# Optimization experiments

Measured on AMD Instinct MI355X. Metric: run time of the kernel, lower is better.

The kernel has to match this reference:

```python
import jax, jax.numpy as jnp
from jax import lax
import numpy as np

T, B, N_INP = 512, 128, 128
N_HID, N_CH, N_OUT, KSIZE = 1024, 2, 10, 3


def setup_inputs() -> dict:
    key = jax.random.key(0)
    ks = jax.random.split(key, 5)
    x = jax.random.normal(ks[0], (T, B, N_INP), jnp.float32)
    # Wx: Linear(n_inp, n_hid*n_ch); original inits std=0.001, scale similarly
    Wx_w = jax.random.normal(ks[1], (N_HID * N_CH, N_INP), jnp.float32) * 0.001
    Wx_b = jnp.zeros((N_HID * N_CH,), jnp.float32)
    # LocallyConnected1d weight [out_ch, in_ch, n_hid, ksize] (leading 1 squeezed)
    Wy_w = jax.random.normal(ks[2], (N_CH, N_CH, N_HID, KSIZE), jnp.float32) * (1.0 / np.sqrt(N_CH * KSIZE))
    Wy_b = jnp.zeros((N_CH, N_HID), jnp.float32)
    R_w = jax.random.normal(ks[3], (N_OUT, N_HID * N_CH), jnp.float32) * (1.0 / np.sqrt(N_HID * N_CH))
    R_b = jnp.zeros((N_OUT,), jnp.float32)
    return {"x": x, "Wx_w": Wx_w, "Wx_b": Wx_b, "Wy_w": Wy_w, "Wy_b": Wy_b, "R_w": R_w, "R_b": R_b}


def reference(x, Wx_w, Wx_b, Wy_w, Wy_b, R_w, R_b):
    n_ch, _, n_hid, ksize = Wy_w.shape
    p = ksize // 2
    # window indices into circularly padded hidden axis (length n_hid + 2p)
    widx = jnp.arange(n_hid)[:, None] + jnp.arange(ksize)[None, :]

    def step(hy, xt):
        # encoder: [B, n_inp] @ [n_inp, n_hid*n_ch]
        u = xt @ Wx_w.T + Wx_b
        h = hy.reshape(-1, n_ch, n_hid)
        # circular pad along hidden dim
        hp = jnp.concatenate([h[..., -p:], h, h[..., :p]], axis=-1)
        win = hp[..., widx]  # [B, n_ch, n_hid, ksize]
        loc = jnp.einsum('bchk,ochk->boh', win, Wy_w) + Wy_b  # [B, n_ch, n_hid]
        hy_new = jnp.tanh(u + loc.reshape(hy.shape[0], n_ch * n_hid))
        return hy_new, None

    hy0 = jnp.zeros((x.shape[1], n_ch * n_hid), x.dtype)
    hy, _ = lax.scan(step, hy0, x)
    return hy @ R_w.T + R_b  # [B, n_out]
```

## Files before the change

### kernel.cpp

```cpp
#include <hip/hip_runtime.h>
#include <hip/hip_bf16.h>

#define T_TOT 512
#define NB    128
#define NI    128
#define NH    1024
#define NJ    2048

typedef __attribute__((ext_vector_type(8))) short short8;
typedef __attribute__((ext_vector_type(4))) float f32x4;
typedef __attribute__((ext_vector_type(2))) float f32x2;

__device__ __forceinline__ unsigned short f2bf_u(float f) {
  __hip_bfloat16 h = __float2bfloat16(f);
  unsigned short s; __builtin_memcpy(&s, &h, 2); return s;
}
__device__ __forceinline__ float bf2f(unsigned short u) {
  unsigned v = ((unsigned)u) << 16; float f; __builtin_memcpy(&f, &v, 4); return f;
}

__global__ void cvt_wx(const float* __restrict__ w,
                       unsigned short* __restrict__ hi,
                       unsigned short* __restrict__ lo) {
  int i = blockIdx.x * blockDim.x + threadIdx.x;
  for (int k = i; k < NJ * NI; k += gridDim.x * blockDim.x) {
    float f = w[k];
    unsigned short h = f2bf_u(f);
    hi[k] = h;
    lo[k] = f2bf_u(f - bf2f(h));
  }
}

__global__ void cvt_x(const float* __restrict__ x,
                      unsigned short* __restrict__ hi,
                      unsigned short* __restrict__ lo) {
  const int n = T_TOT * NB * NI;
  int i = blockIdx.x * blockDim.x + threadIdx.x;
  for (int k = i; k < n; k += gridDim.x * blockDim.x) {
    float f = x[k];
    unsigned short h = f2bf_u(f);
    hi[k] = h;
    lo[k] = f2bf_u(f - bf2f(h));
  }
}

#define MFMA __builtin_amdgcn_mfma_f32_16x16x32_bf16

__global__ __launch_bounds__(256) void fused(
    const unsigned short* __restrict__ xhi,
    const unsigned short* __restrict__ xlo,
    const unsigned short* __restrict__ Whi,
    const unsigned short* __restrict__ Wlo,
    const float* __restrict__ Wxb,
    float* __restrict__ Uw,
    const float* __restrict__ Ur,
    const float* __restrict__ Wyw,
    const float* __restrict__ Wyb,
    const float* __restrict__ Rw,
    const float* __restrict__ Rb,
    float* __restrict__ state,
    float* __restrict__ out,
    int T_c, int nrec, int flags)
{
  __shared__ float edge[2][2][4][2];
  __shared__ float red[4][10];

  if ((int)blockIdx.x < nrec) {
    __builtin_amdgcn_s_setprio(1);
    const int b    = blockIdx.x;
    const int tid  = threadIdx.x;
    const int lane = tid & 63;
    const int wv   = tid >> 6;
    const int n0   = tid * 4;

    f32x2 WP0[12], WP1[12], BP[4];
    {
      const float* w00 = Wyw + (size_t)n0 * 3;
      const float* w01 = Wyw + (size_t)(NH + n0) * 3;
      const float* w10 = Wyw + (size_t)(2 * NH + n0) * 3;
      const float* w11 = Wyw + (size_t)(3 * NH + n0) * 3;
      #pragma unroll
      for (int i = 0; i < 12; ++i) {
        f32x2 a = {w00[i], w10[i]}; WP0[i] = a;
        f32x2 c = {w01[i], w11[i]}; WP1[i] = c;
      }
      #pragma unroll
      for (int j = 0; j < 4; ++j) { f32x2 bb = {Wyb[n0 + j], Wyb[NH + n0 + j]}; BP[j] = bb; }
    }

    float y0[4], y1[4];
    if (flags & 1) {
      #pragma unroll
      for (int j = 0; j < 4; ++j) { y0[j] = 0.f; y1[j] = 0.f; }
    } else {
      float4 s0 = *(const float4*)(state + (size_t)b * NJ + n0);
      float4 s1 = *(const float4*)(state + (size_t)b * NJ + NH + n0);
      y0[0]=s0.x; y0[1]=s0.y; y0[2]=s0.z; y0[3]=s0.w;
      y1[0]=s1.x; y1[1]=s1.y; y1[2]=s1.z; y1[3]=s1.w;
    }

    float lv0, lv1, rv0, rv1;

#define EXCH(P) do {                                                          \
    if (lane == 0)  { edge[P][0][wv][0] = y0[0]; edge[P][0][wv][1] = y1[0]; } \
    if (lane == 63) { edge[P][1][wv][0] = y0[3]; edge[P][1][wv][1] = y1[3]; } \
    lv0 = __shfl(y0[3], (lane + 63) & 63);                                    \
    lv1 = __shfl(y1[3], (lane + 63) & 63);                                    \
    rv0 = __shfl(y0[0], (lane + 1) & 63);                                     \
    rv1 = __shfl(y1[0], (lane + 1) & 63);                                     \
    asm volatile("s_waitcnt lgkmcnt(0)" ::: "memory");                        \
    __builtin_amdgcn_s_barrier();                                             \
    if (lane == 0)  { lv0 = edge[P][1][(wv + 3) & 3][0]; lv1 = edge[P][1][(wv + 3) & 3][1]; } \
    if (lane == 63) { rv0 = edge[P][0][(wv + 1) & 3][0]; rv1 = edge[P][0][(wv + 1) & 3][1]; } \
  } while (0)

#define STEP(P, U0V, U1V) do {                                                \
    float h0[6], h1[6];                                                       \
    h0[0]=lv0; h0[1]=y0[0]; h0[2]=y0[1]; h0[3]=y0[2]; h0[4]=y0[3]; h0[5]=rv0; \
    h1[0]=lv1; h1[1]=y1[0]; h1[2]=y1[1]; h1[3]=y1[2]; h1[4]=y1[3]; h1[5]=rv1; \
    const float u0a[4] = {(U0V).x, (U0V).y, (U0V).z, (U0V).w};                \
    const float u1a[4] = {(U1V).x, (U1V).y, (U1V).z, (U1V).w};                \
    _Pragma("unroll")                                                         \
    for (int j = 0; j < 4; ++j) {                                             \
      f32x2 acc = BP[j];                                                      \
      f32x2 h;                                                                \
      h = (f32x2){h0[j],   h0[j]};   acc = __builtin_elementwise_fma(WP0[j*3+0], h, acc); \
      h = (f32x2){h0[j+1], h0[j+1]}; acc = __builtin_elementwise_fma(WP0[j*3+1], h, acc); \
      h = (f32x2){h0[j+2], h0[j+2]}; acc = __builtin_elementwise_fma(WP0[j*3+2], h, acc); \
      h = (f32x2){h1[j],   h1[j]};   acc = __builtin_elementwise_fma(WP1[j*3+0], h, acc); \
      h = (f32x2){h1[j+1], h1[j+1]}; acc = __builtin_elementwise_fma(WP1[j*3+1], h, acc); \
      h = (f32x2){h1[j+2], h1[j+2]}; acc = __builtin_elementwise_fma(WP1[j*3+2], h, acc); \
      acc += (f32x2){u0a[j], u1a[j]};                                         \
      f32x2 xx = acc * 2.88539008177792681f;   \
      float e0 = __builtin_amdgcn_exp2f(xx.x);                                \
      float e1 = __builtin_amdgcn_exp2f(xx.y);                                \
      y0[j] = fmaf(-2.0f, __builtin_amdgcn_rcpf(e0 + 1.0f), 1.0f);            \
      y1[j] = fmaf(-2.0f, __builtin_amdgcn_rcpf(e1 + 1.0f), 1.0f);            \
    }                                                                         \
    EXCH(P);                                                                  \
  } while (0)

    EXCH(1);

    const float* Ub = Ur + (size_t)b * NJ + n0;
#define LD(S, T) do { const size_t o = (size_t)(T) * ((size_t)NB * NJ);       \
    S##0 = *(const float4*)(Ub + o); S##1 = *(const float4*)(Ub + o + NH); } while (0)

    float4 pA0,pA1,pB0,pB1,pC0,pC1,pD0,pD1,pE0,pE1,pF0,pF1,pG0,pG1,pH0,pH1;
    LD(pA,0); LD(pB,1); LD(pC,2); LD(pD,3); LD(pE,4); LD(pF,5); LD(pG,6); LD(pH,7);

    for (int t = 0; t < T_c; t += 8) {
      STEP(0, pA0, pA1); if (t +  8 < T_c) LD(pA, t +  8);
      STEP(1, pB0, pB1); if (t +  9 < T_c) LD(pB, t +  9);
      STEP(0, pC0, pC1); if (t + 10 < T_c) LD(pC, t + 10);
      STEP(1, pD0, pD1); if (t + 11 < T_c) LD(pD, t + 11);
      STEP(0, pE0, pE1); if (t + 12 < T_c) LD(pE, t + 12);
      STEP(1, pF0, pF1); if (t + 13 < T_c) LD(pF, t + 13);
      STEP(0, pG0, pG1); if (t + 14 < T_c) LD(pG, t + 14);
      STEP(1, pH0, pH1); if (t + 15 < T_c) LD(pH, t + 15);
    }
#undef LD
#undef STEP
#undef EXCH

    if (flags & 2) {
      float p[10];
      #pragma unroll
      for (int r = 0; r < 10; ++r) {
        float4 ra = *(const float4*)(Rw + (size_t)r * NJ + n0);
        float4 rb = *(const float4*)(Rw + (size_t)r * NJ + NH + n0);
        p[r] = y0[0]*ra.x + y0[1]*ra.y + y0[2]*ra.z + y0[3]*ra.w
             + y1[0]*rb.x + y1[1]*rb.y + y1[2]*rb.z + y1[3]*rb.w;
      }
      #pragma unroll
      for (int r = 0; r < 10; ++r) {
        #pragma unroll
        for (int off = 32; off > 0; off >>= 1)
          p[r] += __shfl_down(p[r], off);
      }
      __syncthreads();
      if (lane == 0) {
        #pragma unroll
        for (int r = 0; r < 10; ++r) red[wv][r] = p[r];
      }
      __syncthreads();
      if (tid < 10)
        out[blockIdx.x * 10 + tid] = red[0][tid] + red[1][tid] + red[2][tid] + red[3][tid] + Rb[tid];
    } else {
      *(float4*)(state + (size_t)b * NJ + n0)      = make_float4(y0[0], y0[1], y0[2], y0[3]);
      *(float4*)(state + (size_t)b * NJ + NH + n0) = make_float4(y1[0], y1[1], y1[2], y1[3]);
    }
  } else {
    const int gb = blockIdx.x - nrec;
    const int ts = gb >> 2;
    const int q  = gb & 3;
    const int l  = threadIdx.x & 63;
    const int lr = l & 15;
    const int lk = l >> 4;
    const long m0 = (long)ts * 128 + (threadIdx.x >> 6) * 32;
    const int jb = q * (NJ / 4);

    short8 xh[2][4], xl[2][4];
    #pragma unroll
    for (int ms = 0; ms < 2; ++ms) {
      const size_t base = (size_t)(m0 + ms * 16 + lr) * NI + lk * 8;
      #pragma unroll
      for (int kk = 0; kk < 4; ++kk) {
        xh[ms][kk] = *(const short8*)(xhi + base + kk * 32);
        xl[ms][kk] = *(const short8*)(xlo + base + kk * 32);
      }
    }

#define LOADW(WH, WL, J0) do {                                                \
    const size_t wo = (size_t)((J0) + lr) * NI + lk * 8;                      \
    WH[0] = *(const short8*)(Whi + wo);       WH[1] = *(const short8*)(Whi + wo + 32); \
    WH[2] = *(const short8*)(Whi + wo + 64);  WH[3] = *(const short8*)(Whi + wo + 96); \
    WL[0] = *(const short8*)(Wlo + wo);       WL[1] = *(const short8*)(Wlo + wo + 32); \
    WL[2] = *(const short8*)(Wlo + wo + 64);  WL[3] = *(const short8*)(Wlo + wo + 96); \
  } while (0)

#define COMPUTE(WH, WL, J0) do {                                              \
    f32x4 acc0 = {0.f, 0.f, 0.f, 0.f};                                        \
    f32x4 acc1 = {0.f, 0.f, 0.f, 0.f};                                        \
    _Pragma("unroll")                                                         \
    for (int kk = 0; kk < 4; ++kk) {                                          \
      acc0 = MFMA(WH[kk], xh[0][kk], acc0, 0, 0, 0);                          \
      acc0 = MFMA(WH[kk], xl[0][kk], acc0, 0, 0, 0);                          \
      acc0 = MFMA(WL[kk], xh[0][kk], acc0, 0, 0, 0);                          \
      acc1 = MFMA(WH[kk], xh[1][kk], acc1, 0, 0, 0);                          \
      acc1 = MFMA(WH[kk], xl[1][kk], acc1, 0, 0, 0);                          \
      acc1 = MFMA(WL[kk], xh[1][kk], acc1, 0, 0, 0);                          \
    }                                                                         \
    const float4 b4 = *(const float4*)(Wxb + (J0) + lk * 4);                  \
    float4 o0 = make_float4(acc0[0] + b4.x, acc0[1] + b4.y, acc0[2] + b4.z, acc0[3] + b4.w); \
    float4 o1 = make_float4(acc1[0] + b4.x, acc1[1] + b4.y, acc1[2] + b4.z, acc1[3] + b4.w); \
    *(float4*)(Uw + (m0 + lr) * NJ + (J0) + lk * 4)        = o0;              \
    *(float4*)(Uw + (m0 + 16 + lr) * NJ + (J0) + lk * 4)   = o1;              \
  } while (0)

    short8 whA[4], wlA[4], whB[4], wlB[4];
    LOADW(whA, wlA, jb);
    for (int s = 0; s < 32; s += 2) {
      const int j0 = jb + s * 16;
      LOADW(whB, wlB, j0 + 16);
      COMPUTE(whA, wlA, j0);
      if (s + 2 < 32) LOADW(whA, wlA, j0 + 32);
      COMPUTE(whB, wlB, j0 + 16);
    }
#undef LOADW
#undef COMPUTE
  }
}

__global__ __launch_bounds__(1024) void recur_fb(
    const float* __restrict__ x,
    const float* __restrict__ Wxw, const float* __restrict__ Wxb,
    const float* __restrict__ Wyw, const float* __restrict__ Wyb,
    const float* __restrict__ Rw,  const float* __restrict__ Rb,
    float* __restrict__ out)
{
  const int b = blockIdx.x;
  const int n = threadIdx.x;
  __shared__ float2 h2[2][NH];
  __shared__ float  xs[NI];
  __shared__ float  red[16][10];

  const float w000 = Wyw[(size_t)n*3+0],        w001 = Wyw[(size_t)n*3+1],        w002 = Wyw[(size_t)n*3+2];
  const float w010 = Wyw[(size_t)(NH+n)*3+0],   w011 = Wyw[(size_t)(NH+n)*3+1],   w012 = Wyw[(size_t)(NH+n)*3+2];
  const float w100 = Wyw[(size_t)(2*NH+n)*3+0], w101 = Wyw[(size_t)(2*NH+n)*3+1], w102 = Wyw[(size_t)(2*NH+n)*3+2];
  const float w110 = Wyw[(size_t)(3*NH+n)*3+0], w111 = Wyw[(size_t)(3*NH+n)*3+1], w112 = Wyw[(size_t)(3*NH+n)*3+2];
  const float bias0 = Wyb[n], bias1 = Wyb[NH + n];
  const int nm1 = (n + NH - 1) & (NH - 1);
  const int np1 = (n + 1) & (NH - 1);

  float c0 = 0.f, c1 = 0.f;
  h2[0][n] = make_float2(c0, c1);
  __syncthreads();

  int cur = 0;
  for (int t = 0; t < T_TOT; ++t) {
    if (n < NI) xs[n] = x[(size_t)t * NB * NI + (size_t)b * NI + n];
    __syncthreads();
    float u0 = Wxb[n], u1 = Wxb[NH + n];
    const float* wr0 = Wxw + (size_t)n * NI;
    const float* wr1 = Wxw + (size_t)(NH + n) * NI;
    #pragma unroll 8
    for (int i = 0; i < NI; ++i) {
      u0 = fmaf(xs[i], wr0[i], u0);
      u1 = fmaf(xs[i], wr1[i], u1);
    }
    float2 Lv = h2[cur][nm1];
    float2 Rv = h2[cur][np1];
    float loc0 = bias0 + w000*Lv.x + w001*c0 + w002*Rv.x + w010*Lv.y + w011*c1 + w012*Rv.y;
    float loc1 = bias1 + w100*Lv.x + w101*c0 + w102*Rv.x + w110*Lv.y + w111*c1 + w112*Rv.y;
    float e0 = __expf(2.0f * (u0 + loc0));
    float e1 = __expf(2.0f * (u1 + loc1));
    c0 = 1.0f - __fdividef(2.0f, e0 + 1.0f);
    c1 = 1.0f - __fdividef(2.0f, e1 + 1.0f);
    h2[cur ^ 1][n] = make_float2(c0, c1);
    cur ^= 1;
    __syncthreads();
  }

  float p[10];
  #pragma unroll
  for (int r = 0; r < 10; ++r)
    p[r] = c0 * Rw[(size_t)r * NJ + n] + c1 * Rw[(size_t)r * NJ + NH + n];
  #pragma unroll
  for (int r = 0; r < 10; ++r) {
    #pragma unroll
    for (int off = 32; off > 0; off >>= 1)
      p[r] += __shfl_down(p[r], off);
  }
  const int wv = n >> 6;
  if ((n & 63) == 0) {
    #pragma unroll
    for (int r = 0; r < 10; ++r) red[wv][r] = p[r];
  }
  __syncthreads();
  if (n < 10) {
    float s = 0.f;
    #pragma unroll
    for (int k = 0; k < 16; ++k) s += red[k][n];
    out[b * 10 + n] = s + Rb[n];
  }
}

extern "C" void kernel_launch(void* const* d_in, const int* in_sizes, int n_in,
                              void* d_out, int out_size, void* d_ws, size_t ws_size,
                              hipStream_t stream) {
  const float* x   = (const float*)d_in[0];
  const float* Wxw = (const float*)d_in[1];
  const float* Wxb = (const float*)d_in[2];
  const float* Wyw = (const float*)d_in[3];
  const float* Wyb = (const float*)d_in[4];
  const float* Rw  = (const float*)d_in[5];
  const float* Rb  = (const float*)d_in[6];
  float* out = (float*)d_out;

  const size_t w1_bytes = (size_t)NJ * NI * 2;
  const size_t x1_bytes = (size_t)T_TOT * NB * NI * 2;
  const size_t st_bytes = (size_t)NB * NJ * 4;
  const size_t ut_bytes = (size_t)NB * NJ * 4;

  char* p = (char*)d_ws;
  unsigned short* Whi = (unsigned short*)p;              p += w1_bytes;
  unsigned short* Wlo = (unsigned short*)p;              p += w1_bytes;
  unsigned short* Xhi = (unsigned short*)p;              p += x1_bytes;
  unsigned short* Xlo = (unsigned short*)p;              p += x1_bytes;
  float* state = (float*)p;                              p += st_bytes;
  float* U     = (float*)p;
  const size_t fixed = (size_t)(p - (char*)d_ws);

  long Tc = 64;
  while (Tc >= 8 && fixed + 2 * (size_t)Tc * ut_bytes > ws_size) Tc >>= 1;

  if (Tc >= 8) {
    const int NC = T_TOT / (int)Tc;
    const size_t uhalf = (size_t)Tc * NB * NJ;
    cvt_wx<<<64, 256, 0, stream>>>(Wxw, Whi, Wlo);
    cvt_x<<<1024, 256, 0, stream>>>(x, Xhi, Xlo);
    fused<<<(int)Tc * 4, 256, 0, stream>>>(
        Xhi, Xlo, Whi, Wlo, Wxb, U, nullptr,
        Wyw, Wyb, Rw, Rb, state, out, (int)Tc, 0, 0);
    for (int i = 0; i < NC; ++i) {
      const int flags = (i == 0 ? 1 : 0) | (i == NC - 1 ? 2 : 0);
      const int ng = (i + 1 < NC) ? (int)Tc * 4 : 0;
      const size_t xo = (size_t)(i + 1) * Tc * NB * NI;
      fused<<<128 + ng, 256, 0, stream>>>(
          Xhi + (ng ? xo : 0), Xlo + (ng ? xo : 0), Whi, Wlo, Wxb,
          U + ((size_t)((i + 1) & 1)) * uhalf,
          U + ((size_t)(i & 1)) * uhalf,
          Wyw, Wyb, Rw, Rb, state, out, (int)Tc, 128, flags);
    }
  } else {
    recur_fb<<<NB, 1024, 0, stream>>>(x, Wxw, Wxb, Wyw, Wyb, Rw, Rb, out);
  }
}
```

Baseline: 410.9 us.

## Stage recurrent U prefetch through LDS ring via global_load_lds and split GEMM blocks finer

The recurrent blocks now prefetch the precomputed input projections into a 6-slot LDS ring using direct global-to-LDS loads with explicit vmcnt waits, instead of holding 8 timesteps of float4 registers. This aims to cut register pressure and keep more loads in flight ahead of the serial tanh recurrence. The concurrent GEMM producer blocks are split into 8 column chunks per timestep instead of 4, doubling their count with half the work each. The 48KB LDS ring lowers occupancy for all blocks, including the GEMM blocks that share the kernel, and the hand-written waitcnt counts must match the number of outstanding loads exactly.

After: 430.9 us. 4.9% more time.

```diff
diff --git a/kernel.cpp b/kernel.cpp
--- a/kernel.cpp
+++ b/kernel.cpp
@@ -1,11 +1,13 @@
 #include <hip/hip_runtime.h>
 #include <hip/hip_bf16.h>
+#include <stdint.h>
 
 #define T_TOT 512
 #define NB    128
 #define NI    128
 #define NH    1024
 #define NJ    2048
+#define RING  6
 
 typedef __attribute__((ext_vector_type(8))) short short8;
 typedef __attribute__((ext_vector_type(4))) float f32x4;
@@ -17,6 +19,14 @@
 }
 __device__ __forceinline__ float bf2f(unsigned short u) {
   unsigned v = ((unsigned)u) << 16; float f; __builtin_memcpy(&f, &v, 4); return f;
+}
+
+__device__ __forceinline__ void gl_lds16(const float* g, float* l) {
+  auto* gp = reinterpret_cast<const uint32_t __attribute__((address_space(1)))*>(
+      reinterpret_cast<uintptr_t>(g));
+  auto* lp = reinterpret_cast<uint32_t __attribute__((address_space(3)))*>(
+      (uint32_t)reinterpret_cast<uintptr_t>(l));
+  __builtin_amdgcn_global_load_lds(gp, lp, 16, 0, 0);
 }
 
 __global__ void cvt_wx(const float* __restrict__ w,
@@ -62,6 +72,7 @@
     float* __restrict__ out,
     int T_c, int nrec, int flags)
 {
+  __shared__ float ring[RING * NJ];
   __shared__ float edge[2][2][4][2];
   __shared__ float red[4][10];
 
@@ -131,7 +142,7 @@
       h = (f32x2){h1[j+1], h1[j+1]}; acc = __builtin_elementwise_fma(WP1[j*3+1], h, acc); \
       h = (f32x2){h1[j+2], h1[j+2]}; acc = __builtin_elementwise_fma(WP1[j*3+2], h, acc); \
       acc += (f32x2){u0a[j], u1a[j]};                                         \
-      f32x2 xx = acc * 2.88539008177792681f;   \
+      f32x2 xx = acc * 2.88539008177792681f;                                  \
       float e0 = __builtin_amdgcn_exp2f(xx.x);                                \
       float e1 = __builtin_amdgcn_exp2f(xx.y);                                \
       y0[j] = fmaf(-2.0f, __builtin_amdgcn_rcpf(e0 + 1.0f), 1.0f);            \
@@ -140,26 +151,47 @@
     EXCH(P);                                                                  \
   } while (0)
 
+#define STAGE(TS, SLOT) do {                                                  \
+    int ts_ = (TS); if (ts_ > T_c - 1) ts_ = T_c - 1;                         \
+    const float* grow_ = Ur + ((size_t)ts_ * NB + b) * NJ;                    \
+    float* ls_ = ring + (SLOT) * NJ;                                          \
+    gl_lds16(grow_ + wv * 256 + lane * 4,      ls_ + wv * 256);               \
+    gl_lds16(grow_ + NH + wv * 256 + lane * 4, ls_ + NH + wv * 256);          \
+  } while (0)
+
+    #pragma unroll
+    for (int s = 0; s < RING; ++s) STAGE(s, s);
+    asm volatile("s_waitcnt vmcnt(10)" ::: "memory");
+    __builtin_amdgcn_sched_barrier(0);
+    float4 ucA0, ucA1, ucB0, ucB1;
+    ucA0 = *(const float4*)(ring + 4 * tid);
+    ucA1 = *(const float4*)(ring + NH + 4 * tid);
     EXCH(1);
 
-    const float* Ub = Ur + (size_t)b * NJ + n0;
-#define LD(S, T) do { const size_t o = (size_t)(T) * ((size_t)NB * NJ);       \
-    S##0 = *(const float4*)(Ub + o); S##1 = *(const float4*)(Ub + o + NH); } while (0)
-
-    float4 pA0,pA1,pB0,pB1,pC0,pC1,pD0,pD1,pE0,pE1,pF0,pF1,pG0,pG1,pH0,pH1;
-    LD(pA,0); LD(pB,1); LD(pC,2); LD(pD,3); LD(pE,4); LD(pF,5); LD(pG,6); LD(pH,7);
-
-    for (int t = 0; t < T_c; t += 8) {
-      STEP(0, pA0, pA1); if (t +  8 < T_c) LD(pA, t +  8);
-      STEP(1, pB0, pB1); if (t +  9 < T_c) LD(pB, t +  9);
-      STEP(0, pC0, pC1); if (t + 10 < T_c) LD(pC, t + 10);
-      STEP(1, pD0, pD1); if (t + 11 < T_c) LD(pD, t + 11);
-      STEP(0, pE0, pE1); if (t + 12 < T_c) LD(pE, t + 12);
-      STEP(1, pF0, pF1); if (t + 13 < T_c) LD(pF, t + 13);
-      STEP(0, pG0, pG1); if (t + 14 < T_c) LD(pG, t + 14);
-      STEP(1, pH0, pH1); if (t + 15 < T_c) LD(pH, t + 15);
-    }
-#undef LD
+    int sw = 0, sr = 1;
+    for (int t = 0; t < T_c; t += 2) {
+      STAGE(t + RING, sw); if (++sw == RING) sw = 0;
+      asm volatile("s_waitcnt vmcnt(10)" ::: "memory");
+      __builtin_amdgcn_sched_barrier(0);
+      {
+        const float* rs = ring + sr * NJ;
+        ucB0 = *(const float4*)(rs + 4 * tid);
+        ucB1 = *(const float4*)(rs + NH + 4 * tid);
+        if (++sr == RING) sr = 0;
+      }
+      STEP(0, ucA0, ucA1);
+      STAGE(t + 1 + RING, sw); if (++sw == RING) sw = 0;
+      asm volatile("s_waitcnt vmcnt(10)" ::: "memory");
+      __builtin_amdgcn_sched_barrier(0);
+      {
+        const float* rs = ring + sr * NJ;
+        ucA0 = *(const float4*)(rs + 4 * tid);
+        ucA1 = *(const float4*)(rs + NH + 4 * tid);
+        if (++sr == RING) sr = 0;
+      }
+      STEP(1, ucB0, ucB1);
+    }
+#undef STAGE
 #undef STEP
 #undef EXCH
 
@@ -192,13 +224,12 @@
     }
   } else {
     const int gb = blockIdx.x - nrec;
-    const int ts = gb >> 2;
-    const int q  = gb & 3;
+    const int ts = gb >> 3;
+    const int jb = (gb & 7) * 256;
     const int l  = threadIdx.x & 63;
     const int lr = l & 15;
     const int lk = l >> 4;
     const long m0 = (long)ts * 128 + (threadIdx.x >> 6) * 32;
-    const int jb = q * (NJ / 4);
 
     short8 xh[2][4], xl[2][4];
     #pragma unroll
@@ -240,11 +271,12 @@
 
     short8 whA[4], wlA[4], whB[4], wlB[4];
     LOADW(whA, wlA, jb);
-    for (int s = 0; s < 32; s += 2) {
+    #pragma unroll 2
+    for (int s = 0; s < 16; s += 2) {
       const int j0 = jb + s * 16;
       LOADW(whB, wlB, j0 + 16);
       COMPUTE(whA, wlA, j0);
-      if (s + 2 < 32) LOADW(whA, wlA, j0 + 32);
+      if (s + 2 < 16) LOADW(whA, wlA, j0 + 32);
       COMPUTE(whB, wlB, j0 + 16);
     }
 #undef LOADW
@@ -360,12 +392,12 @@
     const size_t uhalf = (size_t)Tc * NB * NJ;
     cvt_wx<<<64, 256, 0, stream>>>(Wxw, Whi, Wlo);
     cvt_x<<<1024, 256, 0, stream>>>(x, Xhi, Xlo);
-    fused<<<(int)Tc * 4, 256, 0, stream>>>(
+    fused<<<(int)Tc * 8, 256, 0, stream>>>(
         Xhi, Xlo, Whi, Wlo, Wxb, U, nullptr,
         Wyw, Wyb, Rw, Rb, state, out, (int)Tc, 0, 0);
     for (int i = 0; i < NC; ++i) {
       const int flags = (i == 0 ? 1 : 0) | (i == NC - 1 ? 2 : 0);
-      const int ng = (i + 1 < NC) ? (int)Tc * 4 : 0;
+      const int ng = (i + 1 < NC) ? (int)Tc * 8 : 0;
       const size_t xo = (size_t)(i + 1) * Tc * NB * NI;
       fused<<<128 + ng, 256, 0, stream>>>(
           Xhi + (ng ? xo : 0), Xlo + (ng ? xo : 0), Whi, Wlo, Wxb,
```

## Process two batch rows per recurrent block and split GEMM into finer tiles

Applied to the files above, without the earlier changes.

Each recurrent block now handles two batch rows (b and b+64), interleaving their independent tanh-recurrence chains so one barrier per step serves both. This halves the recurrent block count and is meant to hide exp/rcp and barrier latency with ILP. The encoder GEMM side now launches 8 column slices per timestep instead of 4 and does fewer iterations per block. The prefetch depth drops from 8 to 4 steps, and register pressure rises, which could hurt occupancy or latency hiding.

New measurement: 567.2 us. 1.38x slower.

```diff
diff --git a/kernel.cpp b/kernel.cpp
--- a/kernel.cpp
+++ b/kernel.cpp
@@ -1,11 +1,13 @@
 #include <hip/hip_runtime.h>
 #include <hip/hip_bf16.h>
+#include <stdint.h>
 
 #define T_TOT 512
 #define NB    128
 #define NI    128
 #define NH    1024
 #define NJ    2048
+#define NREC  64
 
 typedef __attribute__((ext_vector_type(8))) short short8;
 typedef __attribute__((ext_vector_type(4))) float f32x4;
@@ -62,12 +64,13 @@
     float* __restrict__ out,
     int T_c, int nrec, int flags)
 {
-  __shared__ float edge[2][2][4][2];
-  __shared__ float red[4][10];
+  __shared__ float edge[2][2][4][2][2];
+  __shared__ float red[2][4][10];
 
   if ((int)blockIdx.x < nrec) {
     __builtin_amdgcn_s_setprio(1);
-    const int b    = blockIdx.x;
+    const int b0   = blockIdx.x;
+    const int b1   = b0 + NREC;
     const int tid  = threadIdx.x;
     const int lane = tid & 63;
     const int wv   = tid >> 6;
@@ -88,36 +91,54 @@
       for (int j = 0; j < 4; ++j) { f32x2 bb = {Wyb[n0 + j], Wyb[NH + n0 + j]}; BP[j] = bb; }
     }
 
-    float y0[4], y1[4];
+    float ya0[4], ya1[4], yb0[4], yb1[4];
     if (flags & 1) {
       #pragma unroll
-      for (int j = 0; j < 4; ++j) { y0[j] = 0.f; y1[j] = 0.f; }
+      for (int j = 0; j < 4; ++j) { ya0[j]=0.f; ya1[j]=0.f; yb0[j]=0.f; yb1[j]=0.f; }
     } else {
-      float4 s0 = *(const float4*)(state + (size_t)b * NJ + n0);
-      float4 s1 = *(const float4*)(state + (size_t)b * NJ + NH + n0);
-      y0[0]=s0.x; y0[1]=s0.y; y0[2]=s0.z; y0[3]=s0.w;
-      y1[0]=s1.x; y1[1]=s1.y; y1[2]=s1.z; y1[3]=s1.w;
-    }
-
-    float lv0, lv1, rv0, rv1;
+      float4 s;
+      s = *(const float4*)(state + (size_t)b0 * NJ + n0);      ya0[0]=s.x; ya0[1]=s.y; ya0[2]=s.z; ya0[3]=s.w;
+      s = *(const float4*)(state + (size_t)b0 * NJ + NH + n0); ya1[0]=s.x; ya1[1]=s.y; ya1[2]=s.z; ya1[3]=s.w;
+      s = *(const float4*)(state + (size_t)b1 * NJ + n0);      yb0[0]=s.x; yb0[1]=s.y; yb0[2]=s.z; yb0[3]=s.w;
+      s = *(const float4*)(state + (size_t)b1 * NJ + NH + n0); yb1[0]=s.x; yb1[1]=s.y; yb1[2]=s.z; yb1[3]=s.w;
+    }
+
+    float lva0, lva1, rva0, rva1;
+    float lvb0, lvb1, rvb0, rvb1;
 
 #define EXCH(P) do {                                                          \
-    if (lane == 0)  { edge[P][0][wv][0] = y0[0]; edge[P][0][wv][1] = y1[0]; } \
-    if (lane == 63) { edge[P][1][wv][0] = y0[3]; edge[P][1][wv][1] = y1[3]; } \
-    lv0 = __shfl(y0[3], (lane + 63) & 63);                                    \
-    lv1 = __shfl(y1[3], (lane + 63) & 63);                                    \
-    rv0 = __shfl(y0[0], (lane + 1) & 63);                                     \
-    rv1 = __shfl(y1[0], (lane + 1) & 63);                                     \
+    if (lane == 0) {                                                          \
+      edge[P][0][wv][0][0] = ya0[0]; edge[P][0][wv][0][1] = ya1[0];           \
+      edge[P][0][wv][1][0] = yb0[0]; edge[P][0][wv][1][1] = yb1[0];           \
+    }                                                                         \
+    if (lane == 63) {                                                         \
+      edge[P][1][wv][0][0] = ya0[3]; edge[P][1][wv][0][1] = ya1[3];           \
+      edge[P][1][wv][1][0] = yb0[3]; edge[P][1][wv][1][1] = yb1[3];           \
+    }                                                                         \
+    lva0 = __shfl(ya0[3], (lane + 63) & 63);                                  \
+    lva1 = __shfl(ya1[3], (lane + 63) & 63);                                  \
+    rva0 = __shfl(ya0[0], (lane + 1) & 63);                                   \
+    rva1 = __shfl(ya1[0], (lane + 1) & 63);                                   \
+    lvb0 = __shfl(yb0[3], (lane + 63) & 63);                                  \
+    lvb1 = __shfl(yb1[3], (lane + 63) & 63);                                  \
+    rvb0 = __shfl(yb0[0], (lane + 1) & 63);                                   \
+    rvb1 = __shfl(yb1[0], (lane + 1) & 63);                                   \
     asm volatile("s_waitcnt lgkmcnt(0)" ::: "memory");                        \
     __builtin_amdgcn_s_barrier();                                             \
-    if (lane == 0)  { lv0 = edge[P][1][(wv + 3) & 3][0]; lv1 = edge[P][1][(wv + 3) & 3][1]; } \
-    if (lane == 63) { rv0 = edge[P][0][(wv + 1) & 3][0]; rv1 = edge[P][0][(wv + 1) & 3][1]; } \
+    if (lane == 0) {                                                          \
+      lva0 = edge[P][1][(wv + 3) & 3][0][0]; lva1 = edge[P][1][(wv + 3) & 3][0][1]; \
+      lvb0 = edge[P][1][(wv + 3) & 3][1][0]; lvb1 = edge[P][1][(wv + 3) & 3][1][1]; \
+    }                                                                         \
+    if (lane == 63) {                                                         \
+      rva0 = edge[P][0][(wv + 1) & 3][0][0]; rva1 = edge[P][0][(wv + 1) & 3][0][1]; \
+      rvb0 = edge[P][0][(wv + 1) & 3][1][0]; rvb1 = edge[P][0][(wv + 1) & 3][1][1]; \
+    }                                                                         \
   } while (0)
 
-#define STEP(P, U0V, U1V) do {                                                \
+#define BODY(Y0, Y1, LV0, LV1, RV0, RV1, U0V, U1V) do {                       \
     float h0[6], h1[6];                                                       \
-    h0[0]=lv0; h0[1]=y0[0]; h0[2]=y0[1]; h0[3]=y0[2]; h0[4]=y0[3]; h0[5]=rv0; \
-    h1[0]=lv1; h1[1]=y1[0]; h1[2]=y1[1]; h1[3]=y1[2]; h1[4]=y1[3]; h1[5]=rv1; \
+    h0[0]=LV0; h0[1]=Y0[0]; h0[2]=Y0[1]; h0[3]=Y0[2]; h0[4]=Y0[3]; h0[5]=RV0; \
+    h1[0]=LV1; h1[1]=Y1[0]; h1[2]=Y1[1]; h1[3]=Y1[2]; h1[4]=Y1[3]; h1[5]=RV1; \
     const float u0a[4] = {(U0V).x, (U0V).y, (U0V).z, (U0V).w};                \
     const float u1a[4] = {(U1V).x, (U1V).y, (U1V).z, (U1V).w};                \
     _Pragma("unroll")                                                         \
@@ -131,74 +152,96 @@
       h = (f32x2){h1[j+1], h1[j+1]}; acc = __builtin_elementwise_fma(WP1[j*3+1], h, acc); \
       h = (f32x2){h1[j+2], h1[j+2]}; acc = __builtin_elementwise_fma(WP1[j*3+2], h, acc); \
       acc += (f32x2){u0a[j], u1a[j]};                                         \
-      f32x2 xx = acc * 2.88539008177792681f;   \
+      f32x2 xx = acc * 2.88539008177792681f;                                  \
       float e0 = __builtin_amdgcn_exp2f(xx.x);                                \
       float e1 = __builtin_amdgcn_exp2f(xx.y);                                \
-      y0[j] = fmaf(-2.0f, __builtin_amdgcn_rcpf(e0 + 1.0f), 1.0f);            \
-      y1[j] = fmaf(-2.0f, __builtin_amdgcn_rcpf(e1 + 1.0f), 1.0f);            \
-    }                                                                         \
-    EXCH(P);                                                                  \
+      Y0[j] = fmaf(-2.0f, __builtin_amdgcn_rcpf(e0 + 1.0f), 1.0f);            \
+      Y1[j] = fmaf(-2.0f, __builtin_amdgcn_rcpf(e1 + 1.0f), 1.0f);            \
+    }                                                                         \
   } while (0)
 
+    const float* Ua = Ur + (size_t)b0 * NJ + n0;
+    const float* Ub = Ur + (size_t)b1 * NJ + n0;
+    const size_t sstr = (size_t)NB * NJ;
+#define LDU2(S, T) do {                                                       \
+    int tt_ = (T); if (tt_ > T_c - 1) tt_ = T_c - 1;                          \
+    const size_t o_ = (size_t)tt_ * sstr;                                     \
+    S##a0 = *(const float4*)(Ua + o_); S##a1 = *(const float4*)(Ua + o_ + NH);\
+    S##b0 = *(const float4*)(Ub + o_); S##b1 = *(const float4*)(Ub + o_ + NH);\
+  } while (0)
+
+    float4 pAa0,pAa1,pAb0,pAb1, pBa0,pBa1,pBb0,pBb1;
+    float4 pCa0,pCa1,pCb0,pCb1, pDa0,pDa1,pDb0,pDb1;
+    LDU2(pA, 0); LDU2(pB, 1); LDU2(pC, 2); LDU2(pD, 3);
     EXCH(1);
 
-    const float* Ub = Ur + (size_t)b * NJ + n0;
-#define LD(S, T) do { const size_t o = (size_t)(T) * ((size_t)NB * NJ);       \
-    S##0 = *(const float4*)(Ub + o); S##1 = *(const float4*)(Ub + o + NH); } while (0)
-
-    float4 pA0,pA1,pB0,pB1,pC0,pC1,pD0,pD1,pE0,pE1,pF0,pF1,pG0,pG1,pH0,pH1;
-    LD(pA,0); LD(pB,1); LD(pC,2); LD(pD,3); LD(pE,4); LD(pF,5); LD(pG,6); LD(pH,7);
-
-    for (int t = 0; t < T_c; t += 8) {
-      STEP(0, pA0, pA1); if (t +  8 < T_c) LD(pA, t +  8);
-      STEP(1, pB0, pB1); if (t +  9 < T_c) LD(pB, t +  9);
-      STEP(0, pC0, pC1); if (t + 10 < T_c) LD(pC, t + 10);
-      STEP(1, pD0, pD1); if (t + 11 < T_c) LD(pD, t + 11);
-      STEP(0, pE0, pE1); if (t + 12 < T_c) LD(pE, t + 12);
-      STEP(1, pF0, pF1); if (t + 13 < T_c) LD(pF, t + 13);
-      STEP(0, pG0, pG1); if (t + 14 < T_c) LD(pG, t + 14);
-      STEP(1, pH0, pH1); if (t + 15 < T_c) LD(pH, t + 15);
-    }
-#undef LD
-#undef STEP
+    for (int t = 0; t < T_c; t += 4) {
+      BODY(ya0, ya1, lva0, lva1, rva0, rva1, pAa0, pAa1);
+      BODY(yb0, yb1, lvb0, lvb1, rvb0, rvb1, pAb0, pAb1);
+      LDU2(pA, t + 4);
+      EXCH(0);
+      BODY(ya0, ya1, lva0, lva1, rva0, rva1, pBa0, pBa1);
+      BODY(yb0, yb1, lvb0, lvb1, rvb0, rvb1, pBb0, pBb1);
+      LDU2(pB, t + 5);
+      EXCH(1);
+      BODY(ya0, ya1, lva0, lva1, rva0, rva1, pCa0, pCa1);
+      BODY(yb0, yb1, lvb0, lvb1, rvb0, rvb1, pCb0, pCb1);
+      LDU2(pC, t + 6);
+      EXCH(0);
+      BODY(ya0, ya1, lva0, lva1, rva0, rva1, pDa0, pDa1);
+      BODY(yb0, yb1, lvb0, lvb1, rvb0, rvb1, pDb0, pDb1);
+      LDU2(pD, t + 7);
+      EXCH(1);
+    }
+#undef LDU2
+#undef BODY
 #undef EXCH
 
     if (flags & 2) {
-      float p[10];
+      float pa[10], pb[10];
       #pragma unroll
       for (int r = 0; r < 10; ++r) {
         float4 ra = *(const float4*)(Rw + (size_t)r * NJ + n0);
         float4 rb = *(const float4*)(Rw + (size_t)r * NJ + NH + n0);
-        p[r] = y0[0]*ra.x + y0[1]*ra.y + y0[2]*ra.z + y0[3]*ra.w
-             + y1[0]*rb.x + y1[1]*rb.y + y1[2]*rb.z + y1[3]*rb.w;
+        pa[r] = ya0[0]*ra.x + ya0[1]*ra.y + ya0[2]*ra.z + ya0[3]*ra.w
+              + ya1[0]*rb.x + ya1[1]*rb.y + ya1[2]*rb.z + ya1[3]*rb.w;
+        pb[r] = yb0[0]*ra.x + yb0[1]*ra.y + yb0[2]*ra.z + yb0[3]*ra.w
+              + yb1[0]*rb.x + yb1[1]*rb.y + yb1[2]*rb.z + yb1[3]*rb.w;
       }
       #pragma unroll
       for (int r = 0; r < 10; ++r) {
         #pragma unroll
-        for (int off = 32; off > 0; off >>= 1)
-          p[r] += __shfl_down(p[r], off);
+        for (int off = 32; off > 0; off >>= 1) {
+          pa[r] += __shfl_down(pa[r], off);
+          pb[r] += __shfl_down(pb[r], off);
+        }
       }
       __syncthreads();
       if (lane == 0) {
         #pragma unroll
-        for (int r = 0; r < 10; ++r) red[wv][r] = p[r];
+        for (int r = 0; r < 10; ++r) { red[0][wv][r] = pa[r]; red[1][wv][r] = pb[r]; }
       }
       __syncthreads();
       if (tid < 10)
-        out[blockIdx.x * 10 + tid] = red[0][tid] + red[1][tid] + red[2][tid] + red[3][tid] + Rb[tid];
+        out[b0 * 10 + tid] = red[0][0][tid] + red[0][1][tid] + red[0][2][tid] + red[0][3][tid] + Rb[tid];
+      else if (tid >= 64 && tid < 74) {
+        const int r = tid - 64;
+        out[b1 * 10 + r] = red[1][0][r] + red[1][1][r] + red[1][2][r] + red[1][3][r] + Rb[r];
+      }
     } else {
-      *(float4*)(state + (size_t)b * NJ + n0)      = make_float4(y0[0], y0[1], y0[2], y0[3]);
-      *(float4*)(state + (size_t)b * NJ + NH + n0) = make_float4(y1[0], y1[1], y1[2], y1[3]);
+      *(float4*)(state + (size_t)b0 * NJ + n0)      = make_float4(ya0[0], ya0[1], ya0[2], ya0[3]);
+      *(float4*)(state + (size_t)b0 * NJ + NH + n0) = make_float4(ya1[0], ya1[1], ya1[2], ya1[3]);
+      *(float4*)(state + (size_t)b1 * NJ + n0)      = make_float4(yb0[0], yb0[1], yb0[2], yb0[3]);
+      *(float4*)(state + (size_t)b1 * NJ + NH + n0) = make_float4(yb1[0], yb1[1], yb1[2], yb1[3]);
     }
   } else {
     const int gb = blockIdx.x - nrec;
-    const int ts = gb >> 2;
-    const int q  = gb & 3;
+    const int ts = gb >> 3;
+    const int jb = (gb & 7) * 256;
     const int l  = threadIdx.x & 63;
     const int lr = l & 15;
     const int lk = l >> 4;
     const long m0 = (long)ts * 128 + (threadIdx.x >> 6) * 32;
-    const int jb = q * (NJ / 4);
 
     short8 xh[2][4], xl[2][4];
     #pragma unroll
@@ -219,36 +262,45 @@
     WL[2] = *(const short8*)(Wlo + wo + 64);  WL[3] = *(const short8*)(Wlo + wo + 96); \
   } while (0)
 
-#define COMPUTE(WH, WL, J0) do {                                              \
-    f32x4 acc0 = {0.f, 0.f, 0.f, 0.f};                                        \
-    f32x4 acc1 = {0.f, 0.f, 0.f, 0.f};                                        \
+#define COMPUTEACC(A0, A1, WH, WL) do {                                       \
+    A0 = (f32x4){0.f, 0.f, 0.f, 0.f};                                         \
+    A1 = (f32x4){0.f, 0.f, 0.f, 0.f};                                         \
     _Pragma("unroll")                                                         \
     for (int kk = 0; kk < 4; ++kk) {                                          \
-      acc0 = MFMA(WH[kk], xh[0][kk], acc0, 0, 0, 0);                          \
-      acc0 = MFMA(WH[kk], xl[0][kk], acc0, 0, 0, 0);                          \
-      acc0 = MFMA(WL[kk], xh[0][kk], acc0, 0, 0, 0);                          \
-      acc1 = MFMA(WH[kk], xh[1][kk], acc1, 0, 0, 0);                          \
-      acc1 = MFMA(WH[kk], xl[1][kk], acc1, 0, 0, 0);                          \
-      acc1 = MFMA(WL[kk], xh[1][kk], acc1, 0, 0, 0);                          \
-    }                                                                         \
-    const float4 b4 = *(const float4*)(Wxb + (J0) + lk * 4);                  \
-    float4 o0 = make_float4(acc0[0] + b4.x, acc0[1] + b4.y, acc0[2] + b4.z, acc0[3] + b4.w); \
-    float4 o1 = make_float4(acc1[0] + b4.x, acc1[1] + b4.y, acc1[2] + b4.z, acc1[3] + b4.w); \
-    *(float4*)(Uw + (m0 + lr) * NJ + (J0) + lk * 4)        = o0;              \
-    *(float4*)(Uw + (m0 + 16 + lr) * NJ + (J0) + lk * 4)   = o1;              \
+      A0 = MFMA(WH[kk], xh[0][kk], A0, 0, 0, 0);                              \
+      A0 = MFMA(WH[kk], xl[0][kk], A0, 0, 0, 0);                              \
+      A0 = MFMA(WL[kk], xh[0][kk], A0, 0, 0, 0);                              \
+      A1 = MFMA(WH[kk], xh[1][kk], A1, 0, 0, 0);                              \
+      A1 = MFMA(WH[kk], xl[1][kk], A1, 0, 0, 0);                              \
+      A1 = MFMA(WL[kk], xh[1][kk], A1, 0, 0, 0);                              \
+    }                                                                         \
   } while (0)
 
     short8 whA[4], wlA[4], whB[4], wlB[4];
+    f32x4 aA0, aA1, aB0, aB1;
     LOADW(whA, wlA, jb);
-    for (int s = 0; s < 32; s += 2) {
+    LOADW(whB, wlB, jb + 16);
+    for (int s = 0; s < 16; s += 2) {
       const int j0 = jb + s * 16;
-      LOADW(whB, wlB, j0 + 16);
-      COMPUTE(whA, wlA, j0);
-      if (s + 2 < 32) LOADW(whA, wlA, j0 + 32);
-      COMPUTE(whB, wlB, j0 + 16);
+      COMPUTEACC(aA0, aA1, whA, wlA);
+      if (s + 2 < 16) LOADW(whA, wlA, j0 + 32);
+      COMPUTEACC(aB0, aB1, whB, wlB);
+      if (s + 3 < 16) LOADW(whB, wlB, j0 + 48);
+      const float4 b4a = *(const float4*)(Wxb + j0 + lk * 4);
+      const float4 b4b = *(const float4*)(Wxb + j0 + 16 + lk * 4);
+      float4 oA0 = make_float4(aA0[0]+b4a.x, aA0[1]+b4a.y, aA0[2]+b4a.z, aA0[3]+b4a.w);
+      float4 oB0 = make_float4(aB0[0]+b4b.x, aB0[1]+b4b.y, aB0[2]+b4b.z, aB0[3]+b4b.w);
+      float4 oA1 = make_float4(aA1[0]+b4a.x, aA1[1]+b4a.y, aA1[2]+b4a.z, aA1[3]+b4a.w);
+      float4 oB1 = make_float4(aB1[0]+b4b.x, aB1[1]+b4b.y, aB1[2]+b4b.z, aB1[3]+b4b.w);
+      float* r0 = Uw + (m0 + lr) * NJ + j0 + lk * 4;
+      float* r1 = Uw + (m0 + 16 + lr) * NJ + j0 + lk * 4;
+      *(float4*)(r0)      = oA0;
+      *(float4*)(r0 + 16) = oB0;
+      *(float4*)(r1)      = oA1;
+      *(float4*)(r1 + 16) = oB1;
     }
 #undef LOADW
-#undef COMPUTE
+#undef COMPUTEACC
   }
 }
 
@@ -358,20 +410,21 @@
   if (Tc >= 8) {
     const int NC = T_TOT / (int)Tc;
     const size_t uhalf = (size_t)Tc * NB * NJ;
+    const int ngemm = (int)Tc * 8;
     cvt_wx<<<64, 256, 0, stream>>>(Wxw, Whi, Wlo);
     cvt_x<<<1024, 256, 0, stream>>>(x, Xhi, Xlo);
-    fused<<<(int)Tc * 4, 256, 0, stream>>>(
+    fused<<<ngemm, 256, 0, stream>>>(
         Xhi, Xlo, Whi, Wlo, Wxb, U, nullptr,
         Wyw, Wyb, Rw, Rb, state, out, (int)Tc, 0, 0);
     for (int i = 0; i < NC; ++i) {
       const int flags = (i == 0 ? 1 : 0) | (i == NC - 1 ? 2 : 0);
-      const int ng = (i + 1 < NC) ? (int)Tc * 4 : 0;
+      const int ng = (i + 1 < NC) ? ngemm : 0;
       const size_t xo = (size_t)(i + 1) * Tc * NB * NI;
-      fused<<<128 + ng, 256, 0, stream>>>(
+      fused<<<NREC + ng, 256, 0, stream>>>(
           Xhi + (ng ? xo : 0), Xlo + (ng ? xo : 0), Whi, Wlo, Wxb,
           U + ((size_t)((i + 1) & 1)) * uhalf,
           U + ((size_t)(i & 1)) * uhalf,
-          Wyw, Wyb, Rw, Rb, state, out, (int)Tc, 128, flags);
+          Wyw, Wyb, Rw, Rb, state, out, (int)Tc, NREC, flags);
     }
   } else {
     recur_fb<<<NB, 1024, 0, stream>>>(x, Wxw, Wxb, Wyw, Wyb, Rw, Rb, out);
```

## Map one batch row per wavefront in recurrence, removing block barriers

Applied to the files above, without the earlier changes.

The recurrence now assigns each batch row to a single wavefront, with each lane handling 16 hidden units, so 32 blocks of 4 waves cover the 128 rows. Neighbour exchange then needs only intra-wave shuffles, which removes the LDS edge exchange and the block barrier every timestep. The GEMM side is split into 8 column chunks per timestep instead of 4, launch bounds pin one block per SIMD slot, and the output reduction becomes per-wave. In exchange, per-thread register use grows heavily (96 weight pairs plus 64 prefetched U values), with a risk of spills, and each wave has more serial work per step.

Result: slower. 1.002 ms (+143.8%).

```diff
diff --git a/kernel.cpp b/kernel.cpp
--- a/kernel.cpp
+++ b/kernel.cpp
@@ -1,11 +1,13 @@
 #include <hip/hip_runtime.h>
 #include <hip/hip_bf16.h>
+#include <stdint.h>
 
 #define T_TOT 512
 #define NB    128
 #define NI    128
 #define NH    1024
 #define NJ    2048
+#define NREC  32
 
 typedef __attribute__((ext_vector_type(8))) short short8;
 typedef __attribute__((ext_vector_type(4))) float f32x4;
@@ -46,7 +48,7 @@
 
 #define MFMA __builtin_amdgcn_mfma_f32_16x16x32_bf16
 
-__global__ __launch_bounds__(256) void fused(
+__global__ __launch_bounds__(256, 1) void fused(
     const unsigned short* __restrict__ xhi,
     const unsigned short* __restrict__ xlo,
     const unsigned short* __restrict__ Whi,
@@ -62,66 +64,65 @@
     float* __restrict__ out,
     int T_c, int nrec, int flags)
 {
-  __shared__ float edge[2][2][4][2];
-  __shared__ float red[4][10];
-
   if ((int)blockIdx.x < nrec) {
     __builtin_amdgcn_s_setprio(1);
-    const int b    = blockIdx.x;
     const int tid  = threadIdx.x;
     const int lane = tid & 63;
     const int wv   = tid >> 6;
-    const int n0   = tid * 4;
-
-    f32x2 WP0[12], WP1[12], BP[4];
-    {
-      const float* w00 = Wyw + (size_t)n0 * 3;
-      const float* w01 = Wyw + (size_t)(NH + n0) * 3;
-      const float* w10 = Wyw + (size_t)(2 * NH + n0) * 3;
-      const float* w11 = Wyw + (size_t)(3 * NH + n0) * 3;
-      #pragma unroll
-      for (int i = 0; i < 12; ++i) {
-        f32x2 a = {w00[i], w10[i]}; WP0[i] = a;
-        f32x2 c = {w01[i], w11[i]}; WP1[i] = c;
-      }
-      #pragma unroll
-      for (int j = 0; j < 4; ++j) { f32x2 bb = {Wyb[n0 + j], Wyb[NH + n0 + j]}; BP[j] = bb; }
-    }
-
-    float y0[4], y1[4];
+    const int b    = (int)blockIdx.x * 4 + wv;
+    const int n0   = lane * 16;
+
+    f32x2 WP0[48], WP1[48], BP[16];
+    #pragma unroll
+    for (int j = 0; j < 16; ++j) {
+      const float* w00 = Wyw + (size_t)(n0 + j) * 3;
+      const float* w01 = Wyw + (size_t)(NH + n0 + j) * 3;
+      const float* w10 = Wyw + (size_t)(2 * NH + n0 + j) * 3;
+      const float* w11 = Wyw + (size_t)(3 * NH + n0 + j) * 3;
+      #pragma unroll
+      for (int k = 0; k < 3; ++k) {
+        WP0[j * 3 + k] = (f32x2){w00[k], w10[k]};
+        WP1[j * 3 + k] = (f32x2){w01[k], w11[k]};
+      }
+      BP[j] = (f32x2){Wyb[n0 + j], Wyb[NH + n0 + j]};
+    }
+
+    float y0[16], y1[16];
     if (flags & 1) {
       #pragma unroll
-      for (int j = 0; j < 4; ++j) { y0[j] = 0.f; y1[j] = 0.f; }
+      for (int j = 0; j < 16; ++j) { y0[j] = 0.f; y1[j] = 0.f; }
     } else {
-      float4 s0 = *(const float4*)(state + (size_t)b * NJ + n0);
-      float4 s1 = *(const float4*)(state + (size_t)b * NJ + NH + n0);
-      y0[0]=s0.x; y0[1]=s0.y; y0[2]=s0.z; y0[3]=s0.w;
-      y1[0]=s1.x; y1[1]=s1.y; y1[2]=s1.z; y1[3]=s1.w;
-    }
-
-    float lv0, lv1, rv0, rv1;
-
-#define EXCH(P) do {                                                          \
-    if (lane == 0)  { edge[P][0][wv][0] = y0[0]; edge[P][0][wv][1] = y1[0]; } \
-    if (lane == 63) { edge[P][1][wv][0] = y0[3]; edge[P][1][wv][1] = y1[3]; } \
-    lv0 = __shfl(y0[3], (lane + 63) & 63);                                    \
-    lv1 = __shfl(y1[3], (lane + 63) & 63);                                    \
-    rv0 = __shfl(y0[0], (lane + 1) & 63);                                     \
-    rv1 = __shfl(y1[0], (lane + 1) & 63);                                     \
-    asm volatile("s_waitcnt lgkmcnt(0)" ::: "memory");                        \
-    __builtin_amdgcn_s_barrier();                                             \
-    if (lane == 0)  { lv0 = edge[P][1][(wv + 3) & 3][0]; lv1 = edge[P][1][(wv + 3) & 3][1]; } \
-    if (lane == 63) { rv0 = edge[P][0][(wv + 1) & 3][0]; rv1 = edge[P][0][(wv + 1) & 3][1]; } \
+      #pragma unroll
+      for (int q = 0; q < 4; ++q) {
+        *(float4*)&y0[q * 4] = *(const float4*)(state + (size_t)b * NJ + n0 + q * 4);
+        *(float4*)&y1[q * 4] = *(const float4*)(state + (size_t)b * NJ + NH + n0 + q * 4);
+      }
+    }
+
+    const float* Ubp = Ur + (size_t)b * NJ + n0;
+    const size_t sstr = (size_t)NB * NJ;
+    float uA0[16], uA1[16], uB0[16], uB1[16];
+#define LDU(S0, S1, T) do {                                                   \
+    int tt_ = (T); if (tt_ > T_c - 1) tt_ = T_c - 1;                          \
+    const float* p_ = Ubp + (size_t)tt_ * sstr;                               \
+    _Pragma("unroll")                                                         \
+    for (int q = 0; q < 4; ++q) {                                             \
+      *(float4*)&S0[q * 4] = *(const float4*)(p_ + q * 4);                    \
+      *(float4*)&S1[q * 4] = *(const float4*)(p_ + NH + q * 4);               \
+    }                                                                         \
   } while (0)
 
-#define STEP(P, U0V, U1V) do {                                                \
-    float h0[6], h1[6];                                                       \
-    h0[0]=lv0; h0[1]=y0[0]; h0[2]=y0[1]; h0[3]=y0[2]; h0[4]=y0[3]; h0[5]=rv0; \
-    h1[0]=lv1; h1[1]=y1[0]; h1[2]=y1[1]; h1[3]=y1[2]; h1[4]=y1[3]; h1[5]=rv1; \
-    const float u0a[4] = {(U0V).x, (U0V).y, (U0V).z, (U0V).w};                \
-    const float u1a[4] = {(U1V).x, (U1V).y, (U1V).z, (U1V).w};                \
+#define RSTEP(U0, U1) do {                                                    \
+    float lv0 = __shfl(y0[15], (lane + 63) & 63);                             \
+    float lv1 = __shfl(y1[15], (lane + 63) & 63);                             \
+    float rv0 = __shfl(y0[0],  (lane + 1) & 63);                              \
+    float rv1 = __shfl(y1[0],  (lane + 1) & 63);                              \
+    float h0[18], h1[18];                                                     \
+    h0[0] = lv0; h1[0] = lv1; h0[17] = rv0; h1[17] = rv1;                     \
     _Pragma("unroll")                                                         \
-    for (int j = 0; j < 4; ++j) {                                             \
+    for (int j = 0; j < 16; ++j) { h0[j + 1] = y0[j]; h1[j + 1] = y1[j]; }    \
+    _Pragma("unroll")                                                         \
+    for (int j = 0; j < 16; ++j) {                                            \
       f32x2 acc = BP[j];                                                      \
       f32x2 h;                                                                \
       h = (f32x2){h0[j],   h0[j]};   acc = __builtin_elementwise_fma(WP0[j*3+0], h, acc); \
@@ -130,75 +131,54 @@
       h = (f32x2){h1[j],   h1[j]};   acc = __builtin_elementwise_fma(WP1[j*3+0], h, acc); \
       h = (f32x2){h1[j+1], h1[j+1]}; acc = __builtin_elementwise_fma(WP1[j*3+1], h, acc); \
       h = (f32x2){h1[j+2], h1[j+2]}; acc = __builtin_elementwise_fma(WP1[j*3+2], h, acc); \
-      acc += (f32x2){u0a[j], u1a[j]};                                         \
-      f32x2 xx = acc * 2.88539008177792681f;   \
+      acc += (f32x2){U0[j], U1[j]};                                           \
+      f32x2 xx = acc * 2.88539008177792681f;                                  \
       float e0 = __builtin_amdgcn_exp2f(xx.x);                                \
       float e1 = __builtin_amdgcn_exp2f(xx.y);                                \
       y0[j] = fmaf(-2.0f, __builtin_amdgcn_rcpf(e0 + 1.0f), 1.0f);            \
       y1[j] = fmaf(-2.0f, __builtin_amdgcn_rcpf(e1 + 1.0f), 1.0f);            \
     }                                                                         \
-    EXCH(P);                                                                  \
   } while (0)
 
-    EXCH(1);
-
-    const float* Ub = Ur + (size_t)b * NJ + n0;
-#define LD(S, T) do { const size_t o = (size_t)(T) * ((size_t)NB * NJ);       \
-    S##0 = *(const float4*)(Ub + o); S##1 = *(const float4*)(Ub + o + NH); } while (0)
-
-    float4 pA0,pA1,pB0,pB1,pC0,pC1,pD0,pD1,pE0,pE1,pF0,pF1,pG0,pG1,pH0,pH1;
-    LD(pA,0); LD(pB,1); LD(pC,2); LD(pD,3); LD(pE,4); LD(pF,5); LD(pG,6); LD(pH,7);
-
-    for (int t = 0; t < T_c; t += 8) {
-      STEP(0, pA0, pA1); if (t +  8 < T_c) LD(pA, t +  8);
-      STEP(1, pB0, pB1); if (t +  9 < T_c) LD(pB, t +  9);
-      STEP(0, pC0, pC1); if (t + 10 < T_c) LD(pC, t + 10);
-      STEP(1, pD0, pD1); if (t + 11 < T_c) LD(pD, t + 11);
-      STEP(0, pE0, pE1); if (t + 12 < T_c) LD(pE, t + 12);
-      STEP(1, pF0, pF1); if (t + 13 < T_c) LD(pF, t + 13);
-      STEP(0, pG0, pG1); if (t + 14 < T_c) LD(pG, t + 14);
-      STEP(1, pH0, pH1); if (t + 15 < T_c) LD(pH, t + 15);
-    }
-#undef LD
-#undef STEP
-#undef EXCH
+    LDU(uA0, uA1, 0);
+    LDU(uB0, uB1, 1);
+    for (int t = 0; t < T_c; t += 2) {
+      RSTEP(uA0, uA1); LDU(uA0, uA1, t + 2);
+      RSTEP(uB0, uB1); LDU(uB0, uB1, t + 3);
+    }
+#undef RSTEP
+#undef LDU
 
     if (flags & 2) {
-      float p[10];
       #pragma unroll
       for (int r = 0; r < 10; ++r) {
-        float4 ra = *(const float4*)(Rw + (size_t)r * NJ + n0);
-        float4 rb = *(const float4*)(Rw + (size_t)r * NJ + NH + n0);
-        p[r] = y0[0]*ra.x + y0[1]*ra.y + y0[2]*ra.z + y0[3]*ra.w
-             + y1[0]*rb.x + y1[1]*rb.y + y1[2]*rb.z + y1[3]*rb.w;
-      }
-      #pragma unroll
-      for (int r = 0; r < 10; ++r) {
+        float s = 0.f;
         #pragma unroll
-        for (int off = 32; off > 0; off >>= 1)
-          p[r] += __shfl_down(p[r], off);
-      }
-      __syncthreads();
-      if (lane == 0) {
+        for (int q = 0; q < 4; ++q) {
+          float4 ra = *(const float4*)(Rw + (size_t)r * NJ + n0 + q * 4);
+          float4 rb = *(const float4*)(Rw + (size_t)r * NJ + NH + n0 + q * 4);
+          s += y0[q*4+0]*ra.x + y0[q*4+1]*ra.y + y0[q*4+2]*ra.z + y0[q*4+3]*ra.w;
+          s += y1[q*4+0]*rb.x + y1[q*4+1]*rb.y + y1[q*4+2]*rb.z + y1[q*4+3]*rb.w;
+        }
         #pragma unroll
-        for (int r = 0; r < 10; ++r) red[wv][r] = p[r];
-      }
-      __syncthreads();
-      if (tid < 10)
-        out[blockIdx.x * 10 + tid] = red[0][tid] + red[1][tid] + red[2][tid] + red[3][tid] + Rb[tid];
+        for (int off = 32; off > 0; off >>= 1) s += __shfl_down(s, off);
+        if (lane == 0) out[b * 10 + r] = s + Rb[r];
+      }
     } else {
-      *(float4*)(state + (size_t)b * NJ + n0)      = make_float4(y0[0], y0[1], y0[2], y0[3]);
-      *(float4*)(state + (size_t)b * NJ + NH + n0) = make_float4(y1[0], y1[1], y1[2], y1[3]);
+      #pragma unroll
+      for (int q = 0; q < 4; ++q) {
+        *(float4*)(state + (size_t)b * NJ + n0 + q * 4)      = *(float4*)&y0[q * 4];
+        *(float4*)(state + (size_t)b * NJ + NH + n0 + q * 4) = *(float4*)&y1[q * 4];
+      }
     }
   } else {
     const int gb = blockIdx.x - nrec;
-    const int ts = gb >> 2;
-    const int q  = gb & 3;
+    const int ts = gb >> 3;
+    const int jb = (gb & 7) * 256;
     const int l  = threadIdx.x & 63;
     const int lr = l & 15;
     const int lk = l >> 4;
     const long m0 = (long)ts * 128 + (threadIdx.x >> 6) * 32;
-    const int jb = q * (NJ / 4);
 
     short8 xh[2][4], xl[2][4];
     #pragma unroll
@@ -240,11 +220,12 @@
 
     short8 whA[4], wlA[4], whB[4], wlB[4];
     LOADW(whA, wlA, jb);
-    for (int s = 0; s < 32; s += 2) {
+    #pragma unroll 2
+    for (int s = 0; s < 16; s += 2) {
       const int j0 = jb + s * 16;
       LOADW(whB, wlB, j0 + 16);
       COMPUTE(whA, wlA, j0);
-      if (s + 2 < 32) LOADW(whA, wlA, j0 + 32);
+      if (s + 2 < 16) LOADW(whA, wlA, j0 + 32);
       COMPUTE(whB, wlB, j0 + 16);
     }
 #undef LOADW
@@ -358,20 +339,21 @@
   if (Tc >= 8) {
     const int NC = T_TOT / (int)Tc;
     const size_t uhalf = (size_t)Tc * NB * NJ;
+    const int ngemm = (int)Tc * 8;
     cvt_wx<<<64, 256, 0, stream>>>(Wxw, Whi, Wlo);
     cvt_x<<<1024, 256, 0, stream>>>(x, Xhi, Xlo);
-    fused<<<(int)Tc * 4, 256, 0, stream>>>(
+    fused<<<ngemm, 256, 0, stream>>>(
         Xhi, Xlo, Whi, Wlo, Wxb, U, nullptr,
         Wyw, Wyb, Rw, Rb, state, out, (int)Tc, 0, 0);
     for (int i = 0; i < NC; ++i) {
       const int flags = (i == 0 ? 1 : 0) | (i == NC - 1 ? 2 : 0);
-      const int ng = (i + 1 < NC) ? (int)Tc * 4 : 0;
+      const int ng = (i + 1 < NC) ? ngemm : 0;
       const size_t xo = (size_t)(i + 1) * Tc * NB * NI;
-      fused<<<128 + ng, 256, 0, stream>>>(
+      fused<<<NREC + ng, 256, 0, stream>>>(
           Xhi + (ng ? xo : 0), Xlo + (ng ? xo : 0), Whi, Wlo, Wxb,
           U + ((size_t)((i + 1) & 1)) * uhalf,
           U + ((size_t)(i & 1)) * uhalf,
-          Wyw, Wyb, Rw, Rb, state, out, (int)Tc, 128, flags);
+          Wyw, Wyb, Rw, Rb, state, out, (int)Tc, NREC, flags);
     }
   } else {
     recur_fb<<<NB, 1024, 0, stream>>>(x, Wxw, Wxb, Wyw, Wyb, Rw, Rb, out);
```
